# Optimization experiments

Measured on AMD Instinct MI355X. Metric: run time of the kernel, lower is better.

Reference implementation:

```python
import jax, jax.numpy as jnp
import numpy as np

IN_CH = 64
EMBED = 128
OUT_CH = 64
NUM_HEADS = 2
HEAD_DIM = EMBED // NUM_HEADS
B, D, H, W = 2, 16, 16, 16
SEQ = D * H * W


def setup_inputs() -> dict:
    key = jax.random.key(0)
    ks = jax.random.split(key, 12)
    s = lambda fan_in: 1.0 / np.sqrt(fan_in)
    return {
        "x": jax.random.normal(ks[0], (B, IN_CH, D, H, W), dtype=jnp.float32),
        "W_cp": jax.random.uniform(ks[1], (EMBED, IN_CH), jnp.float32, -s(IN_CH), s(IN_CH)),
        "b_cp": jax.random.uniform(ks[2], (EMBED,), jnp.float32, -s(IN_CH), s(IN_CH)),
        "W_q": jax.random.uniform(ks[3], (EMBED, EMBED), jnp.float32, -s(EMBED), s(EMBED)),
        "W_k": jax.random.uniform(ks[4], (EMBED, EMBED), jnp.float32, -s(EMBED), s(EMBED)),
        "W_v": jax.random.uniform(ks[5], (EMBED, EMBED), jnp.float32, -s(EMBED), s(EMBED)),
        "W_o": jax.random.uniform(ks[6], (EMBED, EMBED), jnp.float32, -s(EMBED), s(EMBED)),
        "b_o": jax.random.uniform(ks[7], (EMBED,), jnp.float32, -s(EMBED), s(EMBED)),
        "W_out": jax.random.uniform(ks[8], (OUT_CH, EMBED), jnp.float32, -s(EMBED), s(EMBED)),
        "b_out": jax.random.uniform(ks[9], (OUT_CH,), jnp.float32, -s(EMBED), s(EMBED)),
        "pos": jax.random.normal(ks[10], (1, SEQ, EMBED), dtype=jnp.float32) * 0.02,
        "gate": jnp.float32(0.1),
    }


def reference(x, W_cp, b_cp, W_q, W_k, W_v, W_o, b_o, W_out, b_out, pos, gate):
    b, c, d, h, w = x.shape
    seq = d * h * w
    scale = HEAD_DIM ** (-0.5)
    # (B, C, D, H, W) -> (B, S, C)
    xf = jnp.transpose(x, (0, 2, 3, 4, 1)).reshape(b, seq, c)
    xf = xf @ W_cp.T + b_cp + pos  # (B, S, E)
    # QKV projections, split heads: (B, nh, S, hd)
    def heads(t):
        return jnp.transpose(t.reshape(b, seq, NUM_HEADS, HEAD_DIM), (0, 2, 1, 3))
    q = heads(xf @ W_q.T)
    k = heads(xf @ W_k.T)
    v = heads(xf @ W_v.T)
    attn = jax.nn.softmax(jnp.einsum("bnsd,bntd->bnst", q, k) * scale, axis=-1)
    o = jnp.einsum("bnst,bntd->bnsd", attn, v)  # (B, nh, S, hd)
    o = jnp.transpose(o, (0, 2, 1, 3)).reshape(b, seq, EMBED)
    o = o @ W_o.T + b_o
    o = o @ W_out.T + b_out  # (B, S, out)
    out = jnp.transpose(o, (0, 2, 1)).reshape(b, OUT_CH, d, h, w)
    # in_channels == output_dim -> skip is identity (no conv/BN in original)
    return out + gate * x
```

## Files before the change

### kernel.cpp

```cpp
#include <hip/hip_runtime.h>
#include <hip/hip_bf16.h>
#include <cstdint>

typedef unsigned short u16;
typedef __attribute__((ext_vector_type(8))) short short8;
typedef __attribute__((ext_vector_type(4))) float f32x4;
typedef __attribute__((ext_vector_type(16))) float f32x16;

#define MFMA(a, b, c) __builtin_amdgcn_mfma_f32_16x16x32_bf16((a), (b), (c), 0, 0, 0)
#define MFMA32(a, b, c) __builtin_amdgcn_mfma_f32_32x32x16_bf16((a), (b), (c), 0, 0, 0)

#define SEQ 4096
#define KSPLIT 8
#define NTILE (SEQ / KSPLIT / 32)

static __device__ __forceinline__ float b2f(u16 u) {
    union { float f; uint32_t i; } c; c.i = ((uint32_t)u) << 16; return c.f;
}
static __device__ __forceinline__ u16 f2b(float f) {
    union { float f; uint32_t i; } c; c.f = f;
    uint32_t r = c.i + 0x7FFF + ((c.i >> 16) & 1);
    return (u16)(r >> 16);
}
static __device__ __forceinline__ short8 ld8(const u16* p) {
    return *reinterpret_cast<const short8*>(p);
}
static __device__ __forceinline__ uint32_t pk2(float a, float b) {
    uint32_t r;
    asm("v_cvt_pk_bf16_f32 %0, %1, %2" : "=v"(r) : "v"(a), "v"(b));
    return r;
}
static __device__ __forceinline__ void plswap(uint32_t& a, uint32_t& b) {
    typedef __attribute__((ext_vector_type(2))) unsigned int u32x2_;
    u32x2_ r = __builtin_amdgcn_permlane32_swap(a, b, false, false);
    a = r[0]; b = r[1];
}
static __device__ __forceinline__ short8 mk8(uint32_t a, uint32_t b, uint32_t c, uint32_t d) {
    union { uint32_t u[4]; short8 s; } cv;
    cv.u[0] = a; cv.u[1] = b; cv.u[2] = c; cv.u[3] = d; return cv.s;
}
static __device__ __forceinline__ short8 ldw8(const float* p) {
    f32x4 a = *reinterpret_cast<const f32x4*>(p);
    f32x4 b = *reinterpret_cast<const f32x4*>(p + 4);
    return mk8(pk2(a[0], a[1]), pk2(a[2], a[3]), pk2(b[0], b[1]), pk2(b[2], b[3]));
}
static __device__ __forceinline__ void gld16(const u16* g, u16* l) {
    __builtin_amdgcn_global_load_lds(
        (const __attribute__((address_space(1))) unsigned int*)g,
        (__attribute__((address_space(3))) unsigned int*)l, 16, 0, 0);
}

__global__ __launch_bounds__(256) void k_front(const float* __restrict__ x,
                                               const float* __restrict__ Wcp,
                                               const float* __restrict__ bcp,
                                               const float* __restrict__ pos,
                                               const float* __restrict__ Wq,
                                               const float* __restrict__ Wk,
                                               const float* __restrict__ Wv,
                                               const float* __restrict__ Wo,
                                               const float* __restrict__ bo,
                                               const float* __restrict__ Wout,
                                               const float* __restrict__ bout,
                                               u16* __restrict__ Q, u16* __restrict__ K,
                                               u16* __restrict__ V,
                                               u16* __restrict__ Wc, float* __restrict__ bc) {
    int blk = blockIdx.x;
    if (blk >= 512) {
        int idx = (blk - 512) * 256 + threadIdx.x;
        if (idx < 8192) {
            int co = idx >> 7, e = idx & 127;
            float s = 0.f;
            for (int k = 0; k < 128; k++)
                s += Wout[co * 128 + k] * Wo[k * 128 + e];
            Wc[idx] = f2b(s);
        } else if (idx < 8256) {
            int co = idx - 8192;
            float s = bout[co];
            for (int k = 0; k < 128; k++)
                s += bo[k] * Wout[co * 128 + k];
            bc[co] = s;
        }
        return;
    }

    __shared__ __align__(16) u16 xT[16][72];
    __shared__ __align__(16) u16 xfl[16 * 128];
    int b = blk >> 8, sb = (blk & 255) * 16;
    int t = threadIdx.x, w = t >> 6, l = t & 63, lc = l & 15, lg = l >> 4;

    {
        int c = t & 63, so = t >> 6;
        const float* src = x + ((size_t)b * 64 + c) * SEQ + sb + so * 4;
        f32x4 a0 = *reinterpret_cast<const f32x4*>(src);
#pragma unroll
        for (int j = 0; j < 4; j++) xT[so * 4 + j][c] = f2b(a0[j]);
    }
    __syncthreads();

    {
        short8 af[2];
        af[0] = ld8(&xT[lc][lg * 8]);
        af[1] = ld8(&xT[lc][32 + lg * 8]);
#pragma unroll
        for (int et = 0; et < 2; et++) {
            int nt = w * 2 + et;
            f32x4 acc = {0.f, 0.f, 0.f, 0.f};
#pragma unroll
            for (int ks = 0; ks < 2; ks++) {
                short8 bfr = ldw8(Wcp + (nt * 16 + lc) * 64 + ks * 32 + lg * 8);
                acc = MFMA(af[ks], bfr, acc);
            }
            int e = nt * 16 + lc;
            float be = bcp[e];
            int chunk = e >> 3;
#pragma unroll
            for (int r = 0; r < 4; r++) {
                int sl = lg * 4 + r;
                float v = acc[r] + be + pos[(size_t)(sb + sl) * 128 + e];
                xfl[sl * 128 + ((chunk ^ (sl & 7)) << 3) + (e & 7)] = f2b(v);
            }
        }
    }
    __syncthreads();

    {
        short8 afq[4];
#pragma unroll
        for (int ks = 0; ks < 4; ks++)
            afq[ks] = ld8(&xfl[lc * 128 + (((ks * 4 + lg) ^ (lc & 7)) << 3)]);

        const float qscl = 0.18033688011112042f;
#pragma unroll
        for (int qk = 0; qk < 2; qk++) {
            const float* W = qk ? Wk : Wq;
            u16* dst = qk ? K : Q;
#pragma unroll
            for (int et = 0; et < 2; et++) {
                int nt = w * 2 + et;
                f32x4 acc = {0.f, 0.f, 0.f, 0.f};
#pragma unroll
                for (int ks = 0; ks < 4; ks++) {
                    short8 bfr = ldw8(W + (nt * 16 + lc) * 128 + ks * 32 + lg * 8);
                    acc = MFMA(afq[ks], bfr, acc);
                }
                int e = nt * 16 + lc, h = e >> 6, d = e & 63;
                float scl = qk ? 1.0f : qscl;
#pragma unroll
                for (int r = 0; r < 4; r++) {
                    int sr = sb + lg * 4 + r;
                    dst[(((size_t)b * 2 + h) * SEQ + sr) * 64 + d] = f2b(acc[r] * scl);
                }
            }
        }
#pragma unroll
        for (int et = 0; et < 2; et++) {
            int nt = w * 2 + et;
            f32x4 acc = {0.f, 0.f, 0.f, 0.f};
            short8 wv[4];
#pragma unroll
            for (int ks = 0; ks < 4; ks++)
                wv[ks] = ldw8(Wv + (nt * 16 + lc) * 128 + ks * 32 + lg * 8);
#pragma unroll
            for (int ks = 0; ks < 4; ks++)
                acc = MFMA(wv[ks], afq[ks], acc);
#pragma unroll
            for (int r = 0; r < 4; r++) {
                int d = nt * 16 + lg * 4 + r, h = d >> 6, dd = d & 63;
                V[((size_t)(b * 2 + h) * 64 + dd) * SEQ + sb + lc] = f2b(acc[r]);
            }
        }
    }
}

__global__ __launch_bounds__(256, 4) void k_attn(const u16* __restrict__ Q,
                                                 const u16* __restrict__ K,
                                                 const u16* __restrict__ Vg,
                                                 u16* __restrict__ Op,
                                                 float* __restrict__ ls) {
    __shared__ __align__(16) u16 Klds[2][2048];
    __shared__ __align__(16) u16 Vlds[2][2048];
    int blk = blockIdx.x;
    int split = blk >> 7, bh = (blk >> 5) & 3, qb = (blk & 31) * 128;
    int kbase = split * (SEQ / KSPLIT);
    const u16* Qp = Q + (size_t)bh * SEQ * 64;
    const u16* Kp = K + (size_t)bh * SEQ * 64;
    const u16* Vp = Vg + (size_t)bh * SEQ * 64;
    int t = threadIdx.x, w = t >> 6, l = t & 63;
    int q = l & 31, hi = l >> 5;

    const u16* kSrc = Kp + (size_t)(kbase + w * 8 + (l >> 3)) * 64 + (((l & 7) ^ (l >> 3)) << 3);
    int vswz = (l & 3) ^ ((((l >> 2) & 3) + (l >> 4)) & 3);
    const u16* vSrc = Vp + (size_t)(w * 16 + (l >> 2)) * SEQ + kbase + (vswz << 3);

    short8 qa[4];
#pragma unroll
    for (int c = 0; c < 4; c++)
        qa[c] = ld8(Qp + (size_t)(qb + w * 32 + q) * 64 + c * 16 + hi * 8);

    short8 onesb;
#pragma unroll
    for (int i = 0; i < 8; i++) onesb[i] = (short)0x3F80;

    f32x16 oaccT[2], lsacc;
#pragma unroll
    for (int i = 0; i < 16; i++) { oaccT[0][i] = 0.f; oaccT[1][i] = 0.f; lsacc[i] = 0.f; }

    int kx = q & 7;
    int sv = ((q & 3) + ((q >> 2) & 3)) & 3;

#define STAGE(buf, tt) do {                                       \
        gld16(kSrc + (size_t)(tt) * 2048, &Klds[buf][w * 512]);   \
        gld16(vSrc + (tt) * 32,           &Vlds[buf][w * 512]);   \
    } while (0)

    STAGE(0, 0);
    __syncthreads();

#pragma unroll 2
    for (int tt = 0; tt < NTILE; tt++) {
        int cur = tt & 1;
        if (tt + 1 < NTILE) STAGE(cur ^ 1, tt + 1);

        const u16* kb = Klds[cur];
        const u16* vb = Vlds[cur];

        f32x16 sc;
#pragma unroll
        for (int i = 0; i < 16; i++) sc[i] = 0.f;
#pragma unroll
        for (int c = 0; c < 4; c++) {
            short8 kf = ld8(kb + q * 64 + ((((c << 1) | hi) ^ kx) << 3));
            sc = MFMA32(kf, qa[c], sc);
        }

        uint32_t pk[8];
#pragma unroll
        for (int j = 0; j < 8; j++)
            pk[j] = pk2(exp2f(sc[2 * j]), exp2f(sc[2 * j + 1]));

        plswap(pk[0], pk[2]); plswap(pk[1], pk[3]);
        plswap(pk[4], pk[6]); plswap(pk[5], pk[7]);
        short8 pA0 = mk8(pk[0], pk[1], pk[2], pk[3]);
        short8 pA1 = mk8(pk[4], pk[5], pk[6], pk[7]);

        lsacc = MFMA32(onesb, pA0, lsacc);
        lsacc = MFMA32(onesb, pA1, lsacc);

#pragma unroll
        for (int dt2 = 0; dt2 < 2; dt2++) {
            short8 va0 = ld8(vb + (dt2 * 32 + q) * 32 + ((hi ^ sv) << 3));
            short8 va1 = ld8(vb + (dt2 * 32 + q) * 32 + (((2 | hi) ^ sv) << 3));
            oaccT[dt2] = MFMA32(va0, pA0, oaccT[dt2]);
            oaccT[dt2] = MFMA32(va1, pA1, oaccT[dt2]);
        }
        __syncthreads();
    }
#undef STAGE

    size_t rowbase = (size_t)(split * 4 + bh) * SEQ + qb + w * 32 + q;
    u16* orow = Op + rowbase * 64;
#pragma unroll
    for (int dt2 = 0; dt2 < 2; dt2++)
#pragma unroll
        for (int i = 0; i < 16; i += 2) {
            int d = dt2 * 32 + (i & 3) + 8 * (i >> 2) + 4 * hi;
            uint32_t wv = pk2(oaccT[dt2][i], oaccT[dt2][i + 1]);
            *reinterpret_cast<uint32_t*>(orow + d) = wv;
        }
    if (hi == 0) ls[rowbase] = lsacc[0];
}

__global__ __launch_bounds__(256) void k_back(const u16* __restrict__ Op,
                                              const float* __restrict__ ls,
                                              const u16* __restrict__ Wc,
                                              const float* __restrict__ bc,
                                              const float* __restrict__ x,
                                              const float* __restrict__ gate,
                                              float* __restrict__ out) {
    __shared__ __align__(16) u16 Ol[16 * 128];
    int blk = blockIdx.x;
    int b = blk >> 8, sb = (blk & 255) * 16;
    int t = threadIdx.x, w = t >> 6, l = t & 63, lc = l & 15, lg = l >> 4;
    float g = gate[0];

    {
        int sl = t >> 4, ci = t & 15;
        int h = ci >> 3, d0 = (ci & 7) * 8;
        size_t rp0 = ((size_t)(b * 2 + h) << 12) + sb + sl;
        float den = 0.f;
#pragma unroll
        for (int k = 0; k < KSPLIT; k++) den += ls[rp0 + (size_t)k * 16384];
        float inv = 1.0f / den;
        float acc[8];
#pragma unroll
        for (int j = 0; j < 8; j++) acc[j] = 0.f;
#pragma unroll
        for (int k = 0; k < KSPLIT; k++) {
            short8 a = ld8(Op + (rp0 + (size_t)k * 16384) * 64 + d0);
#pragma unroll
            for (int j = 0; j < 8; j++) acc[j] += b2f((u16)a[j]);
        }
        short8 ov;
#pragma unroll
        for (int j = 0; j < 8; j++) ov[j] = (short)f2b(acc[j] * inv);
        *reinterpret_cast<short8*>(&Ol[sl * 128 + ((ci ^ (sl & 7)) << 3)]) = ov;
    }
    __syncthreads();

    short8 af[4];
#pragma unroll
    for (int ks = 0; ks < 4; ks++)
        af[ks] = ld8(Wc + (w * 16 + lc) * 128 + ks * 32 + lg * 8);

    f32x4 acc = {0.f, 0.f, 0.f, 0.f};
#pragma unroll
    for (int ks = 0; ks < 4; ks++) {
        short8 bfr = ld8(&Ol[lc * 128 + (((ks * 4 + lg) ^ (lc & 7)) << 3)]);
        acc = MFMA(af[ks], bfr, acc);
    }
#pragma unroll
    for (int r = 0; r < 4; r++) {
        int co = w * 16 + lg * 4 + r;
        int s = sb + lc;
        size_t idx = ((size_t)b * 64 + co) * SEQ + s;
        out[idx] = acc[r] + bc[co] + g * x[idx];
    }
}

extern "C" void kernel_launch(void* const* d_in, const int* in_sizes, int n_in,
                              void* d_out, int out_size, void* d_ws, size_t ws_size,
                              hipStream_t stream) {
    const float* x    = (const float*)d_in[0];
    const float* Wcp  = (const float*)d_in[1];
    const float* bcp  = (const float*)d_in[2];
    const float* Wq   = (const float*)d_in[3];
    const float* Wk   = (const float*)d_in[4];
    const float* Wv   = (const float*)d_in[5];
    const float* Wo   = (const float*)d_in[6];
    const float* bo   = (const float*)d_in[7];
    const float* Wout = (const float*)d_in[8];
    const float* bout = (const float*)d_in[9];
    const float* pos  = (const float*)d_in[10];
    const float* gate = (const float*)d_in[11];

    char* ws = (char*)d_ws;
    float*  lsp  = (float*)(ws);
    u16*    Qb   = (u16*)(ws + (2u << 20));
    u16*    Kb   = (u16*)(ws + (4u << 20));
    u16*    Vt   = (u16*)(ws + (6u << 20));
    u16*    Wc   = (u16*)(ws + (10u << 20));
    float*  bc   = (float*)(ws + (10u << 20) + 16384);
    u16*    Opb  = (u16*)(ws + (10u << 20) + (512u << 10));
    float* out = (float*)d_out;

    hipLaunchKernelGGL(k_front, dim3(545), dim3(256), 0, stream,
                       x, Wcp, bcp, pos, Wq, Wk, Wv, Wo, bo, Wout, bout,
                       Qb, Kb, Vt, Wc, bc);
    hipLaunchKernelGGL(k_attn, dim3(1024), dim3(256), 0, stream, Qb, Kb, Vt, Opb, lsp);
    hipLaunchKernelGGL(k_back, dim3(512), dim3(256), 0, stream, Opb, lsp, Wc, bc, x, gate, out);
}
```

Before: 58.03 us.

## Load K/V fragments directly from global memory instead of LDS staging

Result: slower. 92.32 us (+59.1%).

```diff
diff --git a/kernel.cpp b/kernel.cpp
--- a/kernel.cpp
+++ b/kernel.cpp
@@ -43,11 +43,6 @@
     f32x4 a = *reinterpret_cast<const f32x4*>(p);
     f32x4 b = *reinterpret_cast<const f32x4*>(p + 4);
     return mk8(pk2(a[0], a[1]), pk2(a[2], a[3]), pk2(b[0], b[1]), pk2(b[2], b[3]));
-}
-static __device__ __forceinline__ void gld16(const u16* g, u16* l) {
-    __builtin_amdgcn_global_load_lds(
-        (const __attribute__((address_space(1))) unsigned int*)g,
-        (__attribute__((address_space(3))) unsigned int*)l, 16, 0, 0);
 }
 
 __global__ __launch_bounds__(256) void k_front(const float* __restrict__ x,
@@ -177,8 +172,6 @@
                                                  const u16* __restrict__ Vg,
                                                  u16* __restrict__ Op,
                                                  float* __restrict__ ls) {
-    __shared__ __align__(16) u16 Klds[2][2048];
-    __shared__ __align__(16) u16 Vlds[2][2048];
     int blk = blockIdx.x;
     int split = blk >> 7, bh = (blk >> 5) & 3, qb = (blk & 31) * 128;
     int kbase = split * (SEQ / KSPLIT);
@@ -188,10 +181,6 @@
     int t = threadIdx.x, w = t >> 6, l = t & 63;
     int q = l & 31, hi = l >> 5;
 
-    const u16* kSrc = Kp + (size_t)(kbase + w * 8 + (l >> 3)) * 64 + (((l & 7) ^ (l >> 3)) << 3);
-    int vswz = (l & 3) ^ ((((l >> 2) & 3) + (l >> 4)) & 3);
-    const u16* vSrc = Vp + (size_t)(w * 16 + (l >> 2)) * SEQ + kbase + (vswz << 3);
-
     short8 qa[4];
 #pragma unroll
     for (int c = 0; c < 4; c++)
@@ -205,31 +194,21 @@
 #pragma unroll
     for (int i = 0; i < 16; i++) { oaccT[0][i] = 0.f; oaccT[1][i] = 0.f; lsacc[i] = 0.f; }
 
-    int kx = q & 7;
-    int sv = ((q & 3) + ((q >> 2) & 3)) & 3;
-
-#define STAGE(buf, tt) do {                                       \
-        gld16(kSrc + (size_t)(tt) * 2048, &Klds[buf][w * 512]);   \
-        gld16(vSrc + (tt) * 32,           &Vlds[buf][w * 512]);   \
-    } while (0)
-
-    STAGE(0, 0);
-    __syncthreads();
-
-#pragma unroll 2
+    const u16* kRow  = Kp + (size_t)(kbase + q) * 64 + hi * 8;
+    const u16* vRow0 = Vp + (size_t)q * SEQ + kbase + hi * 8;
+    const u16* vRow1 = Vp + (size_t)(32 + q) * SEQ + kbase + hi * 8;
+
+#pragma unroll 4
     for (int tt = 0; tt < NTILE; tt++) {
-        int cur = tt & 1;
-        if (tt + 1 < NTILE) STAGE(cur ^ 1, tt + 1);
-
-        const u16* kb = Klds[cur];
-        const u16* vb = Vlds[cur];
+        const u16* kb = kRow + (size_t)tt * 32 * 64;
+        int s0 = tt * 32;
 
         f32x16 sc;
 #pragma unroll
         for (int i = 0; i < 16; i++) sc[i] = 0.f;
 #pragma unroll
         for (int c = 0; c < 4; c++) {
-            short8 kf = ld8(kb + q * 64 + ((((c << 1) | hi) ^ kx) << 3));
+            short8 kf = ld8(kb + c * 16);
             sc = MFMA32(kf, qa[c], sc);
         }
 
@@ -243,19 +222,18 @@
         short8 pA0 = mk8(pk[0], pk[1], pk[2], pk[3]);
         short8 pA1 = mk8(pk[4], pk[5], pk[6], pk[7]);
 
+        short8 va00 = ld8(vRow0 + s0);
+        short8 va01 = ld8(vRow0 + s0 + 16);
+        short8 va10 = ld8(vRow1 + s0);
+        short8 va11 = ld8(vRow1 + s0 + 16);
+
         lsacc = MFMA32(onesb, pA0, lsacc);
         lsacc = MFMA32(onesb, pA1, lsacc);
-
-#pragma unroll
-        for (int dt2 = 0; dt2 < 2; dt2++) {
-            short8 va0 = ld8(vb + (dt2 * 32 + q) * 32 + ((hi ^ sv) << 3));
-            short8 va1 = ld8(vb + (dt2 * 32 + q) * 32 + (((2 | hi) ^ sv) << 3));
-            oaccT[dt2] = MFMA32(va0, pA0, oaccT[dt2]);
-            oaccT[dt2] = MFMA32(va1, pA1, oaccT[dt2]);
-        }
-        __syncthreads();
-    }
-#undef STAGE
+        oaccT[0] = MFMA32(va00, pA0, oaccT[0]);
+        oaccT[0] = MFMA32(va01, pA1, oaccT[0]);
+        oaccT[1] = MFMA32(va10, pA0, oaccT[1]);
+        oaccT[1] = MFMA32(va11, pA1, oaccT[1]);
+    }
 
     size_t rowbase = (size_t)(split * 4 + bh) * SEQ + qb + w * 32 + q;
     u16* orow = Op + rowbase * 64;
```
